# Performance work log

Hardware: AMD Instinct MI355X
Metric: run time of the kernel (lower is better)

Reference implementation:

```python
import jax, jax.numpy as jnp
import numpy as np

COMMITMENT_COST = 0.25
NUM_EMBEDDINGS = 1024
EMBEDDING_DIM = 64


def setup_inputs() -> dict:
    key = jax.random.key(0)
    k1, k2 = jax.random.split(key)
    inputs = jax.random.normal(k1, (64, EMBEDDING_DIM, 32, 32), dtype=jnp.float32)
    # nn.Embedding weight init uniform(-1/K, 1/K)
    emb_weight = jax.random.uniform(
        k2, (NUM_EMBEDDINGS, EMBEDDING_DIM), dtype=jnp.float32,
        minval=-1.0 / NUM_EMBEDDINGS, maxval=1.0 / NUM_EMBEDDINGS)
    return {"inputs": inputs, "emb_weight": emb_weight}


def reference(inputs, emb_weight):
    B, C, H, W = inputs.shape  # C == embedding_dim
    K = emb_weight.shape[0]
    # permute to BHWC and flatten to (N, C)
    x = jnp.transpose(inputs, (0, 2, 3, 1)).reshape(-1, C)
    d = (jnp.sum(x * x, axis=1, keepdims=True)
         - 2.0 * (x @ emb_weight.T)
         + jnp.sum(emb_weight * emb_weight, axis=1))  # (N, K)
    idx = jnp.argmin(d, axis=1)  # (N,)
    quantized = emb_weight[idx]  # (N, C) gather

    codebook_loss = jnp.mean((quantized - jax.lax.stop_gradient(x)) ** 2)
    commitment_loss = COMMITMENT_COST * jnp.mean((x - jax.lax.stop_gradient(quantized)) ** 2)
    vq_loss = codebook_loss + commitment_loss

    # straight-through estimator
    quantized_st = x + jax.lax.stop_gradient(quantized - x)
    # NOTE: original torch code does .view(inputs.shape) WITHOUT permuting back
    # from BHWC flat layout; we replicate that exactly for faithfulness.
    quantized_out = quantized_st.reshape(inputs.shape)
    indices_reshaped = idx.reshape(B, H, W)

    # perplexity from codebook usage histogram (equivalent to mean of one-hots)
    counts = jnp.zeros((K,), dtype=inputs.dtype).at[idx].add(1.0)
    avg_probs = counts / x.shape[0]
    perplexity = jnp.exp(-jnp.sum(avg_probs * jnp.log(avg_probs + 1e-10)))

    return quantized_out, vq_loss, indices_reshaped, perplexity
```

## Files before the change

### kernel.cpp

```cpp
#include <hip/hip_runtime.h>
#include <math.h>

#define NUM_K   1024
#define CDIM    64
#define HW      1024
#define NROWS   65536
#define NBLK    1024
#define APAD    200
#define BPAD    224
#define EPS_THR 1.25e-4f
#define RSROWS  16
#define EPADR   68

using bf16x8 = __attribute__((ext_vector_type(8))) short;
using f32x4  = __attribute__((ext_vector_type(4))) float;

__device__ __forceinline__ float np_sumsq64(const float* a) {
#pragma clang fp contract(off)
  float r0 = a[0]*a[0], r1 = a[1]*a[1], r2 = a[2]*a[2], r3 = a[3]*a[3];
  float r4 = a[4]*a[4], r5 = a[5]*a[5], r6 = a[6]*a[6], r7 = a[7]*a[7];
#pragma unroll
  for (int i = 8; i < 64; i += 8) {
    r0 += a[i+0]*a[i+0]; r1 += a[i+1]*a[i+1];
    r2 += a[i+2]*a[i+2]; r3 += a[i+3]*a[i+3];
    r4 += a[i+4]*a[i+4]; r5 += a[i+5]*a[i+5];
    r6 += a[i+6]*a[i+6]; r7 += a[i+7]*a[i+7];
  }
  return ((r0+r1)+(r2+r3))+((r4+r5)+(r6+r7));
}

__global__ void vq_prep(const float* __restrict__ emb, float* __restrict__ norms,
                        unsigned short* __restrict__ esp)
{
  const int k = blockIdx.x * blockDim.x + threadIdx.x;
  if (k >= NUM_K) return;
  norms[k] = np_sumsq64(emb + k * CDIM);
  unsigned short* row = esp + (size_t)k * BPAD;
  for (int c = 0; c < CDIM; ++c) {
    const float v = emb[k * CDIM + c];
    const unsigned int vb = __float_as_uint(v);
    const unsigned short h = (unsigned short)(vb >> 16);
    const float res = v - __uint_as_float((unsigned int)h << 16);
    const unsigned short l = (unsigned short)(__float_as_uint(res) >> 16);
    row[c] = h; row[64 + c] = h; row[128 + c] = l;
  }
  for (int i = 192; i < BPAD; ++i) row[i] = 0;
}

__global__ __launch_bounds__(256, 2)
void vq_dist(const float* __restrict__ xin, const float* __restrict__ norms,
             const unsigned short* __restrict__ esp, float* __restrict__ out_idx,
             unsigned int* __restrict__ nflag, unsigned int* __restrict__ flaglist)
{
  __shared__ __align__(16) unsigned short A_s[64 * APAD];
  __shared__ float red_m1[4][64];
  __shared__ float red_m2[4][64];

  const int t    = threadIdx.x;
  const int lane = t & 63;
  const int w    = t >> 6;
  const int l15  = lane & 15;
  const int g4   = lane >> 4;

  const int n0  = blockIdx.x * 64;
  const int b   = n0 >> 10;
  const int hw0 = n0 & (HW - 1);

  {
    const int r = t & 63, q = t >> 6;
    const float* xb = xin + (size_t)b * (CDIM * HW) + hw0 + r;
    unsigned short* arow = A_s + r * APAD;
#pragma unroll
    for (int u = 0; u < 8; ++u) {
      const int c0 = q * 16 + 2 * u;
      const float v0 = xb[(size_t)c0 * HW];
      const float v1 = xb[(size_t)(c0 + 1) * HW];
      const unsigned int h0 = __float_as_uint(v0) >> 16;
      const unsigned int h1 = __float_as_uint(v1) >> 16;
      const float r0 = v0 - __uint_as_float(h0 << 16);
      const float r1 = v1 - __uint_as_float(h1 << 16);
      const unsigned int lo0 = __float_as_uint(r0) >> 16;
      const unsigned int lo1 = __float_as_uint(r1) >> 16;
      const unsigned int hh = h0 | (h1 << 16);
      const unsigned int ll = lo0 | (lo1 << 16);
      *(unsigned int*)(arow + c0)        = hh;
      *(unsigned int*)(arow + 64 + c0)   = ll;
      *(unsigned int*)(arow + 128 + c0)  = hh;
    }
  }
  __syncthreads();

  float m1[16], m2[16];
#pragma unroll
  for (int i = 0; i < 16; ++i) { m1[i] = INFINITY; m2[i] = INFINITY; }

  const unsigned short* aF = A_s + l15 * APAD + g4 * 8;
  const unsigned short* pB = esp + (size_t)(w * 32 + l15) * BPAD + g4 * 8;
  const float* pN = norms + w * 32 + l15;

  bf16x8 c0 = *(const bf16x8*)(pB);
  bf16x8 c1 = *(const bf16x8*)(pB + 16 * BPAD);

#pragma unroll 1
  for (int cb = 0; cb < 8; ++cb) {
    const float nk0 = pN[0];
    const float nk1 = pN[16];

    f32x4 acc[4][2];
#pragma unroll
    for (int rt = 0; rt < 4; ++rt)
#pragma unroll
      for (int ct = 0; ct < 2; ++ct)
        acc[rt][ct] = (f32x4){0.0f, 0.0f, 0.0f, 0.0f};

    {
      const bf16x8 a0 = *(const bf16x8*)(aF);
      const bf16x8 a1 = *(const bf16x8*)(aF + 16 * APAD);
      const bf16x8 a2 = *(const bf16x8*)(aF + 32 * APAD);
      const bf16x8 a3 = *(const bf16x8*)(aF + 48 * APAD);
      acc[0][0] = __builtin_amdgcn_mfma_f32_16x16x32_bf16(a0, c0, acc[0][0], 0, 0, 0);
      acc[1][0] = __builtin_amdgcn_mfma_f32_16x16x32_bf16(a1, c0, acc[1][0], 0, 0, 0);
      acc[2][0] = __builtin_amdgcn_mfma_f32_16x16x32_bf16(a2, c0, acc[2][0], 0, 0, 0);
      acc[3][0] = __builtin_amdgcn_mfma_f32_16x16x32_bf16(a3, c0, acc[3][0], 0, 0, 0);
      acc[0][1] = __builtin_amdgcn_mfma_f32_16x16x32_bf16(a0, c1, acc[0][1], 0, 0, 0);
      acc[1][1] = __builtin_amdgcn_mfma_f32_16x16x32_bf16(a1, c1, acc[1][1], 0, 0, 0);
      acc[2][1] = __builtin_amdgcn_mfma_f32_16x16x32_bf16(a2, c1, acc[2][1], 0, 0, 0);
      acc[3][1] = __builtin_amdgcn_mfma_f32_16x16x32_bf16(a3, c1, acc[3][1], 0, 0, 0);
    }
#pragma unroll
    for (int s = 1; s < 6; ++s) {
      const bf16x8 b0 = *(const bf16x8*)(pB + s * 32);
      const bf16x8 b1 = *(const bf16x8*)(pB + 16 * BPAD + s * 32);
      const bf16x8 a0 = *(const bf16x8*)(aF + s * 32);
      const bf16x8 a1 = *(const bf16x8*)(aF + 16 * APAD + s * 32);
      const bf16x8 a2 = *(const bf16x8*)(aF + 32 * APAD + s * 32);
      const bf16x8 a3 = *(const bf16x8*)(aF + 48 * APAD + s * 32);
      acc[0][0] = __builtin_amdgcn_mfma_f32_16x16x32_bf16(a0, b0, acc[0][0], 0, 0, 0);
      acc[1][0] = __builtin_amdgcn_mfma_f32_16x16x32_bf16(a1, b0, acc[1][0], 0, 0, 0);
      acc[2][0] = __builtin_amdgcn_mfma_f32_16x16x32_bf16(a2, b0, acc[2][0], 0, 0, 0);
      acc[3][0] = __builtin_amdgcn_mfma_f32_16x16x32_bf16(a3, b0, acc[3][0], 0, 0, 0);
      acc[0][1] = __builtin_amdgcn_mfma_f32_16x16x32_bf16(a0, b1, acc[0][1], 0, 0, 0);
      acc[1][1] = __builtin_amdgcn_mfma_f32_16x16x32_bf16(a1, b1, acc[1][1], 0, 0, 0);
      acc[2][1] = __builtin_amdgcn_mfma_f32_16x16x32_bf16(a2, b1, acc[2][1], 0, 0, 0);
      acc[3][1] = __builtin_amdgcn_mfma_f32_16x16x32_bf16(a3, b1, acc[3][1], 0, 0, 0);
    }

    const unsigned kbase = (unsigned)(cb * 128 + w * 32 + l15);
    pB += 128 * BPAD;
    pN += 128;
    c0 = *(const bf16x8*)(pB);
    c1 = *(const bf16x8*)(pB + 16 * BPAD);

#pragma unroll
    for (int ct = 0; ct < 2; ++ct) {
      const float nk = ct ? nk1 : nk0;
      const unsigned kcol = kbase + (unsigned)(ct * 16);
#pragma unroll
      for (int rt = 0; rt < 4; ++rt) {
#pragma unroll
        for (int rg = 0; rg < 4; ++rg) {
          const float g  = fmaf(-2.0f, acc[rt][ct][rg], nk);
          const float gp = __uint_as_float((__float_as_uint(g) & 0xFFFFFC00u) | kcol);
          const int   si = rt * 4 + rg;
          m2[si] = fminf(m2[si], fmaxf(m1[si], gp));
          m1[si] = fminf(m1[si], gp);
        }
      }
    }
  }

#pragma unroll
  for (int mask = 1; mask <= 8; mask <<= 1) {
#pragma unroll
    for (int si = 0; si < 16; ++si) {
      const float om1 = __shfl_xor(m1[si], mask, 64);
      const float om2 = __shfl_xor(m2[si], mask, 64);
      m2[si] = fminf(fminf(m2[si], om2), fmaxf(m1[si], om1));
      m1[si] = fminf(m1[si], om1);
    }
  }
  if (l15 == 0) {
#pragma unroll
    for (int rt = 0; rt < 4; ++rt)
#pragma unroll
      for (int rg = 0; rg < 4; ++rg) {
        const int row = rt * 16 + g4 * 4 + rg;
        red_m1[w][row] = m1[rt * 4 + rg];
        red_m2[w][row] = m2[rt * 4 + rg];
      }
  }
  __syncthreads();
  if (t < 64) {
    float M1 = red_m1[0][t], M2 = red_m2[0][t];
#pragma unroll
    for (int ww = 1; ww < 4; ++ww) {
      const float om1 = red_m1[ww][t], om2 = red_m2[ww][t];
      M2 = fminf(fminf(M2, om2), fmaxf(M1, om1));
      M1 = fminf(M1, om1);
    }
    const int K1 = (int)(__float_as_uint(M1) & 1023u);
    out_idx[n0 + t] = (float)K1;
    if (M2 - M1 <= EPS_THR) {
      const unsigned pos = atomicAdd(nflag, 1u);
      flaglist[pos] = (unsigned)(n0 + t);
    }
  }
}

__global__ __launch_bounds__(256)
void vq_rescan(const float* __restrict__ xin, const float* __restrict__ emb,
               const float* __restrict__ norms,
               const unsigned int* __restrict__ nflag,
               const unsigned int* __restrict__ flaglist,
               float* __restrict__ out_idx)
{
  __shared__ __align__(16) float e_s[128 * EPADR];
  __shared__ float x_s[RSROWS * EPADR];
  const int t  = threadIdx.x;
  const int rr = t >> 4;
  const int tk = t & 15;
  const unsigned nf = *nflag;

  for (unsigned base = blockIdx.x * RSROWS; base < nf; base += gridDim.x * RSROWS) {
    const unsigned ridx  = base + (unsigned)rr;
    const bool     active = ridx < nf;
    const int n  = (int)flaglist[active ? ridx : (nf - 1)];
    const int bb = n >> 10, hw = n & (HW - 1);

    {
      const float* xb = xin + (size_t)bb * (CDIM * HW) + hw;
#pragma unroll
      for (int j = 0; j < 4; ++j) {
        const int c = tk * 4 + j;
        x_s[rr * EPADR + c] = xb[(size_t)c * HW];
      }
    }
    __syncthreads();

    float xr[CDIM];
#pragma unroll
    for (int c = 0; c < CDIM; ++c) xr[c] = x_s[rr * EPADR + c];
    const float S = np_sumsq64(xr);

    float dmin = INFINITY; int kmin = 0;

    for (int cb = 0; cb < 8; ++cb) {
      __syncthreads();
      {
        const float4* src = (const float4*)(emb + (size_t)cb * 128 * CDIM);
#pragma unroll
        for (int i = 0; i < 8; ++i) {
          const int f    = i * 256 + t;
          const int code = f >> 4, c4 = f & 15;
          *(float4*)(e_s + code * EPADR + c4 * 4) = src[f];
        }
      }
      __syncthreads();

#pragma unroll 2
      for (int j = 0; j < 8; ++j) {
        const int kk = j * 16 + tk;
        const float* er = e_s + kk * EPADR;
        float d = 0.0f;
#pragma unroll
        for (int c4 = 0; c4 < 16; ++c4) {
          const float4 a = *(const float4*)(er + 4 * c4);
          d = fmaf(xr[4*c4+0], a.x, d);
          d = fmaf(xr[4*c4+1], a.y, d);
          d = fmaf(xr[4*c4+2], a.z, d);
          d = fmaf(xr[4*c4+3], a.w, d);
        }
        const int k = cb * 128 + kk;
        const float q = (S - 2.0f * d) + norms[k];
        if (q < dmin) { dmin = q; kmin = k; }
      }
    }

#pragma unroll
    for (int mask = 1; mask <= 8; mask <<= 1) {
      const float od = __shfl_xor(dmin, mask, 64);
      const int   ok = __shfl_xor(kmin, mask, 64);
      if (od < dmin || (od == dmin && ok < kmin)) { dmin = od; kmin = ok; }
    }
    if (active && tk == 0) out_idx[n] = (float)kmin;
    __syncthreads();
  }
}

__global__ __launch_bounds__(64)
void vq_epilogue(const float* __restrict__ xin, const float* __restrict__ emb,
                 const float* __restrict__ out_idx, float* __restrict__ out0,
                 double* __restrict__ partials, unsigned int* __restrict__ counts)
{
  __shared__ unsigned int hist_s[NUM_K];
  const int t = threadIdx.x;
  const int n = blockIdx.x * 64 + t;
  for (int i = t; i < NUM_K; i += 64) hist_s[i] = 0;
  __syncthreads();
  const int bb = n >> 10, hw = n & (HW - 1);
  const float* xb = xin + (size_t)bb * (CDIM * HW) + hw;
  int kmin = (int)out_idx[n];
  if (kmin < 0) kmin = 0;
  atomicAdd(&hist_s[kmin], 1u);
  const float4* eb = (const float4*)(emb + (size_t)kmin * CDIM);
  float4* o = (float4*)(out0 + (size_t)n * CDIM);
  float ssq = 0.0f;
#pragma unroll
  for (int c4 = 0; c4 < 16; ++c4) {
    const float4 q4 = eb[c4];
    const float x0 = xb[(4*c4+0) * HW], x1 = xb[(4*c4+1) * HW];
    const float x2 = xb[(4*c4+2) * HW], x3 = xb[(4*c4+3) * HW];
    const float u0 = q4.x - x0, u1 = q4.y - x1, u2 = q4.z - x2, u3 = q4.w - x3;
    ssq = fmaf(u0, u0, fmaf(u1, u1, fmaf(u2, u2, fmaf(u3, u3, ssq))));
    o[c4] = make_float4(x0 + u0, x1 + u1, x2 + u2, x3 + u3);
  }
#pragma unroll
  for (int off = 32; off > 0; off >>= 1) ssq += __shfl_down(ssq, off, 64);
  if (t == 0) partials[blockIdx.x] = (double)ssq;
  __syncthreads();
  for (int i = t; i < NUM_K; i += 64) {
    const unsigned int v = hist_s[i];
    if (v) atomicAdd(&counts[i], v);
  }
}

__global__ void vq_final(const double* __restrict__ partials,
                         const unsigned int* __restrict__ counts,
                         float* __restrict__ out_loss, float* __restrict__ out_perp)
{
  __shared__ double sh[256];
  const int t = threadIdx.x;
  double acc = 0.0, ent = 0.0;
  for (int i = t; i < NBLK; i += 256) acc += partials[i];
  for (int k = t; k < NUM_K; k += 256) {
    const double pr = (double)counts[k] * (1.0 / 65536.0);
    ent += pr * log(pr + 1e-10);
  }
  sh[t] = acc;
  __syncthreads();
  for (int s = 128; s > 0; s >>= 1) { if (t < s) sh[t] += sh[t + s]; __syncthreads(); }
  const double total = sh[0];
  __syncthreads();
  sh[t] = ent;
  __syncthreads();
  for (int s = 128; s > 0; s >>= 1) { if (t < s) sh[t] += sh[t + s]; __syncthreads(); }
  if (t == 0) {
    out_loss[0] = (float)(1.25 * total / 4194304.0);
    out_perp[0] = (float)exp(-sh[0]);
  }
}

extern "C" void kernel_launch(void* const* d_in, const int* in_sizes, int n_in,
                              void* d_out, int out_size, void* d_ws, size_t ws_size,
                              hipStream_t stream)
{
  const float* xin = (const float*)d_in[0];
  const float* emb = (const float*)d_in[1];
  float* out = (float*)d_out;

  float*        norms    = (float*)d_ws;
  unsigned int* counts   = (unsigned int*)((char*)d_ws + 4096);
  double*       partials = (double*)((char*)d_ws + 8192);

  float* out0     = out;
  float* out_loss = out + 4194304;
  float* out_idx  = out + 4194305;
  float* out_perp = out + 4194305 + 65536;

  unsigned short* esp      = (unsigned short*)out0;
  unsigned int*   nflag    = (unsigned int*)((char*)out0 + (8u << 20));
  unsigned int*   flaglist = nflag + 1;

  hipMemsetAsync((char*)d_ws + 4096, 0, 4096, stream);
  hipMemsetAsync(nflag, 0, 4, stream);

  vq_prep    <<<dim3(16),   dim3(64),  0, stream>>>(emb, norms, esp);
  vq_dist    <<<dim3(1024), dim3(256), 0, stream>>>(xin, norms, esp, out_idx,
                                                    nflag, flaglist);
  vq_rescan  <<<dim3(512),  dim3(256), 0, stream>>>(xin, emb, norms, nflag,
                                                    flaglist, out_idx);
  vq_epilogue<<<dim3(1024), dim3(64),  0, stream>>>(xin, emb, out_idx, out0, partials, counts);
  vq_final   <<<dim3(1),    dim3(256), 0, stream>>>(partials, counts, out_loss, out_perp);
}
```

Measured before the change: 208.2 us.

## Split rescan across codebook chunks with packed-min partials and a reduce kernel

The exact fp32 rescan of flagged rows is split so each block handles one 16-row group against one 128-code chunk instead of looping over all 8 chunks, and the grid grows from 512 to 2048 blocks. Each block writes a packed (order-preserving distance bits, index) 64-bit partial, and a new small kernel takes the minimum of the 8 partials per row to write the final index. The aim is more parallelism when few rows are flagged. The cost is one extra kernel launch, the x rows being reloaded 8 times, and a partial buffer placed inside the output scratch area.

```diff
diff --git a/kernel.cpp b/kernel.cpp
--- a/kernel.cpp
+++ b/kernel.cpp
@@ -9,7 +9,6 @@
 #define APAD    200
 #define BPAD    224
 #define EPS_THR 1.25e-4f
-#define RSROWS  16
 #define EPADR   68
 
 using bf16x8 = __attribute__((ext_vector_type(8))) short;
@@ -212,20 +211,25 @@
                const float* __restrict__ norms,
                const unsigned int* __restrict__ nflag,
                const unsigned int* __restrict__ flaglist,
-               float* __restrict__ out_idx)
+               unsigned long long* __restrict__ pmin)
 {
   __shared__ __align__(16) float e_s[128 * EPADR];
-  __shared__ float x_s[RSROWS * EPADR];
+  __shared__ float x_s[16 * EPADR];
   const int t  = threadIdx.x;
   const int rr = t >> 4;
   const int tk = t & 15;
   const unsigned nf = *nflag;
-
-  for (unsigned base = blockIdx.x * RSROWS; base < nf; base += gridDim.x * RSROWS) {
-    const unsigned ridx  = base + (unsigned)rr;
+  const unsigned T  = ((nf + 15) >> 4) * 8u;
+
+  for (unsigned tau = blockIdx.x; tau < T; tau += gridDim.x) {
+    const unsigned g  = tau >> 3;
+    const int      cb = (int)(tau & 7);
+    const unsigned ridx   = g * 16 + (unsigned)rr;
     const bool     active = ridx < nf;
     const int n  = (int)flaglist[active ? ridx : (nf - 1)];
     const int bb = n >> 10, hw = n & (HW - 1);
+
+    __syncthreads();
 
     {
       const float* xb = xin + (size_t)bb * (CDIM * HW) + hw;
@@ -235,6 +239,15 @@
         x_s[rr * EPADR + c] = xb[(size_t)c * HW];
       }
     }
+    {
+      const float4* src = (const float4*)(emb + (size_t)cb * 128 * CDIM);
+#pragma unroll
+      for (int i = 0; i < 8; ++i) {
+        const int f    = i * 256 + t;
+        const int code = f >> 4, c4 = f & 15;
+        *(float4*)(e_s + code * EPADR + c4 * 4) = src[f];
+      }
+    }
     __syncthreads();
 
     float xr[CDIM];
@@ -243,37 +256,22 @@
     const float S = np_sumsq64(xr);
 
     float dmin = INFINITY; int kmin = 0;
-
-    for (int cb = 0; cb < 8; ++cb) {
-      __syncthreads();
-      {
-        const float4* src = (const float4*)(emb + (size_t)cb * 128 * CDIM);
-#pragma unroll
-        for (int i = 0; i < 8; ++i) {
-          const int f    = i * 256 + t;
-          const int code = f >> 4, c4 = f & 15;
-          *(float4*)(e_s + code * EPADR + c4 * 4) = src[f];
-        }
+#pragma unroll 2
+    for (int j = 0; j < 8; ++j) {
+      const int kk = j * 16 + tk;
+      const float* er = e_s + kk * EPADR;
+      float d = 0.0f;
+#pragma unroll
+      for (int c4 = 0; c4 < 16; ++c4) {
+        const float4 a = *(const float4*)(er + 4 * c4);
+        d = fmaf(xr[4*c4+0], a.x, d);
+        d = fmaf(xr[4*c4+1], a.y, d);
+        d = fmaf(xr[4*c4+2], a.z, d);
+        d = fmaf(xr[4*c4+3], a.w, d);
       }
-      __syncthreads();
-
-#pragma unroll 2
-      for (int j = 0; j < 8; ++j) {
-        const int kk = j * 16 + tk;
-        const float* er = e_s + kk * EPADR;
-        float d = 0.0f;
-#pragma unroll
-        for (int c4 = 0; c4 < 16; ++c4) {
-          const float4 a = *(const float4*)(er + 4 * c4);
-          d = fmaf(xr[4*c4+0], a.x, d);
-          d = fmaf(xr[4*c4+1], a.y, d);
-          d = fmaf(xr[4*c4+2], a.z, d);
-          d = fmaf(xr[4*c4+3], a.w, d);
-        }
-        const int k = cb * 128 + kk;
-        const float q = (S - 2.0f * d) + norms[k];
-        if (q < dmin) { dmin = q; kmin = k; }
-      }
+      const int k = cb * 128 + kk;
+      const float q = (S - 2.0f * d) + norms[k];
+      if (q < dmin) { dmin = q; kmin = k; }
     }
 
 #pragma unroll
@@ -282,8 +280,29 @@
       const int   ok = __shfl_xor(kmin, mask, 64);
       if (od < dmin || (od == dmin && ok < kmin)) { dmin = od; kmin = ok; }
     }
-    if (active && tk == 0) out_idx[n] = (float)kmin;
-    __syncthreads();
+    if (active && tk == 0) {
+      const float dc = dmin + 0.0f;
+      unsigned mb = __float_as_uint(dc);
+      mb = (mb & 0x80000000u) ? ~mb : (mb | 0x80000000u);
+      pmin[(size_t)ridx * 8 + cb] =
+          ((unsigned long long)mb << 32) | (unsigned long long)(unsigned)kmin;
+    }
+  }
+}
+
+__global__ void vq_resfin(const unsigned int* __restrict__ nflag,
+                          const unsigned int* __restrict__ flaglist,
+                          const unsigned long long* __restrict__ pmin,
+                          float* __restrict__ out_idx)
+{
+  const unsigned nf = *nflag;
+  for (unsigned i = blockIdx.x * blockDim.x + threadIdx.x; i < nf;
+       i += gridDim.x * blockDim.x) {
+    const unsigned long long* p = pmin + (size_t)i * 8;
+    unsigned long long m = p[0];
+#pragma unroll
+    for (int j = 1; j < 8; ++j) { const unsigned long long v = p[j]; m = v < m ? v : m; }
+    out_idx[flaglist[i]] = (float)(unsigned)(m & 1023u);
   }
 }
 
@@ -367,9 +386,10 @@
   float* out_idx  = out + 4194305;
   float* out_perp = out + 4194305 + 65536;
 
-  unsigned short* esp      = (unsigned short*)out0;
-  unsigned int*   nflag    = (unsigned int*)((char*)out0 + (8u << 20));
-  unsigned int*   flaglist = nflag + 1;
+  unsigned short*     esp      = (unsigned short*)out0;
+  unsigned int*       nflag    = (unsigned int*)((char*)out0 + (8u << 20));
+  unsigned int*       flaglist = nflag + 1;
+  unsigned long long* pmin     = (unsigned long long*)((char*)out0 + (10u << 20));
 
   hipMemsetAsync((char*)d_ws + 4096, 0, 4096, stream);
   hipMemsetAsync(nflag, 0, 4, stream);
@@ -377,8 +397,9 @@
   vq_prep    <<<dim3(16),   dim3(64),  0, stream>>>(emb, norms, esp);
   vq_dist    <<<dim3(1024), dim3(256), 0, stream>>>(xin, norms, esp, out_idx,
                                                     nflag, flaglist);
-  vq_rescan  <<<dim3(512),  dim3(256), 0, stream>>>(xin, emb, norms, nflag,
-                                                    flaglist, out_idx);
+  vq_rescan  <<<dim3(2048), dim3(256), 0, stream>>>(xin, emb, norms, nflag,
+                                                    flaglist, pmin);
+  vq_resfin  <<<dim3(64),   dim3(256), 0, stream>>>(nflag, flaglist, pmin, out_idx);
   vq_epilogue<<<dim3(1024), dim3(64),  0, stream>>>(xin, emb, out_idx, out0, partials, counts);
   vq_final   <<<dim3(1),    dim3(256), 0, stream>>>(partials, counts, out_loss, out_perp);
 }
```

After: 184.7 us. -11.3%, faster.
